# Optimization experiments

Measured on AMD Instinct MI355X. Metric: run time of the kernel, lower is better.

## Reference

```python
import jax, jax.numpy as jnp
import numpy as np

B, T, D, H, TE = 8, 1024, 1024, 16, 2048  # batch, seq, latent_dim, heads, time_embed_dim
LN_EPS = 1e-5


def layer_norm(x, w, b):
    m = jnp.mean(x, axis=-1, keepdims=True)
    v = jnp.var(x, axis=-1, keepdims=True)
    return (x - m) / jnp.sqrt(v + LN_EPS) * w + b


def setup_inputs() -> dict:
    key = jax.random.key(0)
    ks = jax.random.split(key, 8)
    s = lambda k, sh: (jax.random.normal(k, sh, jnp.float32) * 0.02)
    return dict(
        x=jax.random.normal(ks[0], (B, T, D), jnp.float32),
        emb=jax.random.normal(ks[1], (B, TE), jnp.float32),
        src_mask=jnp.ones((B, T), jnp.float32),
        norm_w=jnp.ones((D,), jnp.float32), norm_b=jnp.zeros((D,), jnp.float32),
        q_w=s(ks[2], (D, D)), q_b=jnp.zeros((D,), jnp.float32),
        k_w=s(ks[3], (D, D)), k_b=jnp.zeros((D,), jnp.float32),
        v_w=s(ks[4], (D, D)), v_b=jnp.zeros((D,), jnp.float32),
        emb_w=s(ks[5], (TE, 2 * D)), emb_b=jnp.zeros((2 * D,), jnp.float32),
        sb_norm_w=jnp.ones((D,), jnp.float32), sb_norm_b=jnp.zeros((D,), jnp.float32),
        out_w=s(ks[6], (D, D)), out_b=jnp.zeros((D,), jnp.float32),
    )


def reference(x, emb, src_mask, norm_w, norm_b, q_w, q_b, k_w, k_b, v_w, v_b,
              emb_w, emb_b, sb_norm_w, sb_norm_b, out_w, out_b):
    Bx, Tx, Dx = x.shape
    # the torch module applies the SAME LayerNorm to x three times; compute once
    xn = layer_norm(x, norm_w, norm_b)                      # [B,T,D]
    q = (xn @ q_w + q_b).reshape(Bx, Tx, H, -1)             # [B,T,H,l]
    k = (xn @ k_w + k_b).reshape(Bx, Tx, H, -1)
    att = jnp.einsum('bnhl,bmhl->bnmh', q, k)               # [B,T,T,H] (no 1/sqrt(d) scaling, as in source)
    mask = src_mask.reshape(Bx, 1, Tx, 1)
    att = att + (1.0 - mask) * -1000000.0
    att = jax.nn.softmax(att, axis=2)                       # softmax over keys (dim m)
    v = ((xn @ v_w + v_b) * src_mask[:, :, None]).reshape(Bx, Tx, H, -1)
    y = jnp.einsum('bnmh,bmhl->bnhl', att, v).reshape(Bx, Tx, Dx)
    # StylizationBlock (dropout is identity in eval)
    e = jax.nn.silu(emb) @ emb_w + emb_b                    # [B,2D]
    scale, shift = jnp.split(e[:, None, :], 2, axis=2)      # each [B,1,D]
    h = layer_norm(y, sb_norm_w, sb_norm_b) * (1.0 + scale) + shift
    h = jax.nn.silu(h) @ out_w + out_b
    return x + h
```

## Files before the change

### kernel.cpp

```cpp
#include <hip/hip_runtime.h>
#include <cstddef>
#include <cstdint>

#define B_SZ 8
#define T_SEQ 1024
#define D_MODEL 1024
#define NH 16
#define HD 64
#define TE_DIM 2048
#define BT_ROWS 8192

typedef short bf16x8 __attribute__((ext_vector_type(8)));
typedef float f32x4 __attribute__((ext_vector_type(4)));

#define MFMA16(a, b, c) __builtin_amdgcn_mfma_f32_16x16x32_bf16(a, b, c, 0, 0, 0)
#define EXP2(x) __builtin_amdgcn_exp2f(x)

__device__ inline unsigned short f2b(float f) {
  union { float f; unsigned u; } v; v.f = f;
  unsigned r = v.u + 0x7FFF + ((v.u >> 16) & 1);
  return (unsigned short)(r >> 16);
}

__device__ inline float b2f(unsigned short u) {
  union { unsigned u; float f; } v; v.u = ((unsigned)u) << 16; return v.f;
}

__device__ inline unsigned cvtpk(float a, float b) {
  unsigned r;
  asm("v_cvt_pk_bf16_f32 %0, %1, %2" : "=v"(r) : "v"(a), "v"(b));
  return r;
}

__device__ inline void gll16(const void* g, void* l) {
  __builtin_amdgcn_global_load_lds(
      (const __attribute__((address_space(1))) unsigned int*)g,
      (__attribute__((address_space(3))) unsigned int*)l, 16, 0, 0);
}

__global__ __launch_bounds__(256) void ln_kernel(
    const float* __restrict__ x, const float* __restrict__ w,
    const float* __restrict__ b, unsigned short* __restrict__ out)
{
  __shared__ float red[8];
  int row = blockIdx.x;
  int tid = threadIdx.x;
  const float* xr = x + (size_t)row * D_MODEL;
  float4 xv = *(const float4*)&xr[tid * 4];
  float s  = xv.x + xv.y + xv.z + xv.w;
  float ss = xv.x*xv.x + xv.y*xv.y + xv.z*xv.z + xv.w*xv.w;
  #pragma unroll
  for (int off = 32; off; off >>= 1) {
    s  += __shfl_xor(s, off);
    ss += __shfl_xor(ss, off);
  }
  int wv = tid >> 6;
  if ((tid & 63) == 0) { red[wv] = s; red[4 + wv] = ss; }
  __syncthreads();
  s  = red[0] + red[1] + red[2] + red[3];
  ss = red[4] + red[5] + red[6] + red[7];
  float mean = s * (1.f / D_MODEL);
  float var  = ss * (1.f / D_MODEL) - mean * mean;
  float inv  = rsqrtf(var + 1e-5f);
  float4 w4 = *(const float4*)&w[tid * 4];
  float4 b4 = *(const float4*)&b[tid * 4];
  ushort4 o;
  o.x = f2b((xv.x - mean) * inv * w4.x + b4.x);
  o.y = f2b((xv.y - mean) * inv * w4.y + b4.y);
  o.z = f2b((xv.z - mean) * inv * w4.z + b4.z);
  o.w = f2b((xv.w - mean) * inv * w4.w + b4.w);
  int kg = tid >> 4, cb = (tid >> 1) & 7, e = (tid & 1) * 4;
  int col = kg * 64 + ((cb ^ (row & 7)) * 8) + e;
  *(ushort4*)&out[(size_t)row * D_MODEL + col] = o;
}

__global__ __launch_bounds__(256) void transpose_w4(
    const float* __restrict__ s0, const float* __restrict__ s1,
    const float* __restrict__ s2, const float* __restrict__ s3,
    unsigned short* __restrict__ d0, unsigned short* __restrict__ d1,
    unsigned short* __restrict__ d2, unsigned short* __restrict__ d3)
{
  __shared__ float s[32][33];
  int z = blockIdx.z;
  const float* in = z == 0 ? s0 : z == 1 ? s1 : z == 2 ? s2 : s3;
  unsigned short* out = z == 0 ? d0 : z == 1 ? d1 : z == 2 ? d2 : d3;
  int tx = threadIdx.x & 31, ty = threadIdx.x >> 5;
  int r0 = blockIdx.y * 32, c0 = blockIdx.x * 32;
  #pragma unroll
  for (int rr = 0; rr < 4; ++rr)
    s[ty + rr * 8][tx] = in[(size_t)(r0 + ty + rr * 8) * D_MODEL + c0 + tx];
  __syncthreads();
  int k = r0 + tx;
  int kg = k >> 6, cb = (k >> 3) & 7, e = k & 7;
  #pragma unroll
  for (int rr = 0; rr < 4; ++rr) {
    int n = c0 + ty + rr * 8;
    int col = kg * 64 + ((cb ^ (n & 7)) * 8) + e;
    out[(size_t)n * D_MODEL + col] = f2b(s[tx][ty + rr * 8]);
  }
}

template <int MODE>
__global__ __launch_bounds__(512, 2) void gemm8(
    const unsigned short* __restrict__ A, const unsigned short* __restrict__ W,
    const float* __restrict__ b0, const float* __restrict__ b1,
    const float* __restrict__ b2, const float* __restrict__ mask,
    const float* __restrict__ resid, void* __restrict__ C)
{
  const int K = 1024;
  __shared__ __align__(16) unsigned short SA[3][256 * 64];
  __shared__ __align__(16) unsigned short SB[3][128 * 64];
  int tid = threadIdx.x;
  int wid = tid >> 6, lane = tid & 63, g = lane >> 4, lq = lane & 15;
  int wm = wid >> 1, wn = wid & 1;
  int bid = blockIdx.x;
  int xcd = bid & 7, ii = bid >> 3;
  int mt = xcd * 4 + (ii & 3), nt = ii >> 2;
  int m0 = mt * 256;
  int wg = (MODE == 1) ? (nt >> 3) : 0;
  int n0 = (MODE == 1) ? ((nt & 7) * 128) : (nt * 128);
  const unsigned short* Bt = W + ((size_t)wg << 20);
  const float* bias = (MODE == 1) ? (wg == 0 ? b0 : wg == 1 ? b1 : b2) : b0;

  f32x4 acc[4][4];
  #pragma unroll
  for (int i = 0; i < 4; ++i)
    #pragma unroll
    for (int j = 0; j < 4; ++j)
      acc[i][j] = (f32x4){0.f, 0.f, 0.f, 0.f};

  const unsigned short* aSrc = A + (size_t)(m0 + (tid >> 3)) * K + (tid & 7) * 8;
  const unsigned short* bSrc = Bt + (size_t)(n0 + (tid >> 3)) * K + (tid & 7) * 8;

  #define STAGE8(slot, t)                                                      \
    {                                                                          \
      size_t ko = (size_t)(t) * 64;                                            \
      _Pragma("unroll")                                                        \
      for (int i2 = 0; i2 < 4; ++i2)                                           \
        gll16(aSrc + ko + (size_t)i2 * 64 * K,                                 \
              (char*)&SA[slot][0] + tid * 16 + i2 * 8192);                     \
      _Pragma("unroll")                                                        \
      for (int i2 = 0; i2 < 2; ++i2)                                           \
        gll16(bSrc + ko + (size_t)i2 * 64 * K,                                 \
              (char*)&SB[slot][0] + tid * 16 + i2 * 8192);                     \
    }

  STAGE8(0, 0)
  STAGE8(1, 1)
  asm volatile("s_waitcnt vmcnt(6)" ::: "memory");
  asm volatile("s_barrier" ::: "memory");

  int cA0 = (g ^ (lq & 7)) * 16;
  int cA1 = ((4 + g) ^ (lq & 7)) * 16;

  #pragma unroll
  for (int t = 0; t < 16; ++t) {
    const char* sa = (const char*)&SA[t % 3][0];
    const char* sb = (const char*)&SB[t % 3][0];
    bf16x8 af[4][2], bf[4][2];
    #pragma unroll
    for (int i = 0; i < 4; ++i) {
      int ra = wm * 64 + i * 16 + lq;
      af[i][0] = *(const bf16x8*)(sa + ra * 128 + cA0);
      af[i][1] = *(const bf16x8*)(sa + ra * 128 + cA1);
      int rb = wn * 64 + i * 16 + lq;
      bf[i][0] = *(const bf16x8*)(sb + rb * 128 + cA0);
      bf[i][1] = *(const bf16x8*)(sb + rb * 128 + cA1);
    }
    if (t < 14) {
      STAGE8((t + 2) % 3, t + 2)
      asm volatile("s_waitcnt vmcnt(6)" ::: "memory");
    } else if (t == 14) {
      asm volatile("s_waitcnt vmcnt(0)" ::: "memory");
    }
    __builtin_amdgcn_s_setprio(1);
    #pragma unroll
    for (int i = 0; i < 4; ++i)
      #pragma unroll
      for (int j = 0; j < 4; ++j) {
        acc[i][j] = MFMA16(af[i][0], bf[j][0], acc[i][j]);
        acc[i][j] = MFMA16(af[i][1], bf[j][1], acc[i][j]);
      }
    __builtin_amdgcn_s_setprio(0);
    if (t < 15) asm volatile("s_barrier" ::: "memory");
  }
  #undef STAGE8

  int colbase = n0 + wn * 64;
  #pragma unroll
  for (int i = 0; i < 4; ++i) {
    int mrow0 = m0 + wm * 64 + i * 16 + g * 4;
    #pragma unroll
    for (int j = 0; j < 4; ++j) {
      int n = colbase + j * 16 + lq;
      float bv = bias[n];
      if (MODE == 0) {
        float* Cf = (float*)C;
        #pragma unroll
        for (int rr = 0; rr < 4; ++rr) {
          int m = mrow0 + rr;
          Cf[(size_t)m * D_MODEL + n] = acc[i][j][rr] + bv + resid[(size_t)m * D_MODEL + n];
        }
      } else {
        int h = n >> 6, dd = n & 63;
        unsigned short* O = (unsigned short*)C;
        if (wg < 2) {
          float scale = wg == 0 ? 1.44269504f : 1.0f;
          unsigned short* Cb = O + ((size_t)wg << 23);
          #pragma unroll
          for (int rr = 0; rr < 4; ++rr) {
            int m = mrow0 + rr;
            int b = m >> 10, tt = m & 1023;
            Cb[((size_t)((b * NH + h) * T_SEQ + tt)) * HD + dd] = f2b((acc[i][j][rr] + bv) * scale);
          }
        } else {
          unsigned short* Cb = O + ((size_t)2 << 23);
          int b = mrow0 >> 10, tt = mrow0 & 1023;
          ushort4 pk;
          unsigned short* pp = (unsigned short*)&pk;
          #pragma unroll
          for (int rr = 0; rr < 4; ++rr)
            pp[rr] = f2b((acc[i][j][rr] + bv) * mask[mrow0 + rr]);
          *(ushort4*)&Cb[((size_t)((b * NH + h) * HD + dd)) * T_SEQ + tt] = pk;
        }
      }
    }
  }
}

__global__ __launch_bounds__(256) void emb_partial(
    const float* __restrict__ emb, const float* __restrict__ emb_w,
    float* __restrict__ partial)
{
  __shared__ float ses[B_SZ][32];
  int tid = threadIdx.x;
  int t0 = blockIdx.y * 32;
  int n = blockIdx.x * 1024 + tid * 4;
  {
    int b = tid >> 5, t = tid & 31;
    float v = emb[b * TE_DIM + t0 + t];
    ses[b][t] = v / (1.f + __expf(-v));
  }
  __syncthreads();
  f32x4 acc[B_SZ];
  #pragma unroll
  for (int b = 0; b < B_SZ; ++b) acc[b] = (f32x4){0.f, 0.f, 0.f, 0.f};
  #pragma unroll 4
  for (int t = 0; t < 32; ++t) {
    f32x4 wv = *(const f32x4*)&emb_w[(size_t)(t0 + t) * (2 * D_MODEL) + n];
    #pragma unroll
    for (int b = 0; b < B_SZ; ++b) {
      float s = ses[b][t];
      acc[b][0] = fmaf(s, wv[0], acc[b][0]);
      acc[b][1] = fmaf(s, wv[1], acc[b][1]);
      acc[b][2] = fmaf(s, wv[2], acc[b][2]);
      acc[b][3] = fmaf(s, wv[3], acc[b][3]);
    }
  }
  #pragma unroll
  for (int b = 0; b < B_SZ; ++b)
    *(f32x4*)&partial[((size_t)blockIdx.y * B_SZ + b) * (2 * D_MODEL) + n] = acc[b];
}

__global__ __launch_bounds__(256) void emb_reduce(
    const float* __restrict__ partial, const float* __restrict__ emb_b,
    float* __restrict__ e)
{
  int idx = blockIdx.x * 256 + threadIdx.x;
  int b = idx >> 11, n = idx & 2047;
  float acc = emb_b[n];
  #pragma unroll 8
  for (int kb = 0; kb < 64; ++kb)
    acc += partial[((size_t)kb * B_SZ + b) * (2 * D_MODEL) + n];
  e[b * (2 * D_MODEL) + n] = acc;
}

__global__ __launch_bounds__(256, 2) void attn_mfma6(
    const unsigned short* __restrict__ Q, const unsigned short* __restrict__ K,
    const unsigned short* __restrict__ Vt, const float* __restrict__ mask,
    unsigned short* __restrict__ y)
{
  __shared__ __align__(16) unsigned short SM[32768];
  unsigned short* Kb = SM;
  unsigned short* Vb = SM + 8192;
  unsigned short* Pb = SM + 16384;

  int tid = threadIdx.x, w = tid >> 6, lane = tid & 63;
  int g = lane >> 4, lq = lane & 15;
  int bid = blockIdx.x;
  int lid = (bid & 7) * 64 + (bid >> 3);
  int qb = lid & 3, h = (lid >> 2) & 15, b = lid >> 6;
  int q0 = qb * 256 + w * 64;
  size_t hb = ((size_t)(b * NH + h)) * T_SEQ * HD;

  bf16x8 bq[4][2];
  #pragma unroll
  for (int qa = 0; qa < 4; ++qa)
    #pragma unroll
    for (int kh = 0; kh < 2; ++kh)
      bq[qa][kh] = *(const bf16x8*)(Q + hb + (size_t)(q0 + qa * 16 + lq) * HD + kh * 32 + g * 8);

  const char* kBase = (const char*)(K + hb) + lq * 128 + g * 16;
  const char* vBase = (const char*)(Vt + hb) + lq * 2048 + g * 16;
  int c0 = 2 * w, c1 = 2 * w + 1;
  const char* kS0 = kBase + (c0 >> 1) * 2048 + (c0 & 1) * 64;
  const char* kS1 = kBase + (c1 >> 1) * 2048 + (c1 & 1) * 64;
  const char* vS0 = vBase + (c0 >> 1) * 32768 + (c0 & 1) * 64;
  const char* vS1 = vBase + (c1 >> 1) * 32768 + (c1 & 1) * 64;

  f32x4 o[4][4];
  #pragma unroll
  for (int dt = 0; dt < 4; ++dt)
    #pragma unroll
    for (int qa = 0; qa < 4; ++qa)
      o[dt][qa] = (f32x4){0.f, 0.f, 0.f, 0.f};
  float mrun[4] = {-3.0e38f, -3.0e38f, -3.0e38f, -3.0e38f};
  float lrun[4] = {0.f, 0.f, 0.f, 0.f};
  const float* maskb = mask + b * T_SEQ;

  gll16(kS0, Kb + c0 * 512);
  gll16(kS1, Kb + c1 * 512);
  gll16(vS0, Vb + c0 * 512);
  gll16(vS1, Vb + c1 * 512);
  __syncthreads();

  for (int t = 0; t < 16; ++t) {
    int cur = t & 1;
    int kv0 = t * 64;
    if (t < 15) {
      int nxt = cur ^ 1;
      size_t ko = (size_t)(kv0 + 64) * 128;
      size_t vo = (size_t)(kv0 + 64) * 2;
      gll16(kS0 + ko, Kb + nxt * 4096 + c0 * 512);
      gll16(kS1 + ko, Kb + nxt * 4096 + c1 * 512);
      gll16(vS0 + vo, Vb + nxt * 4096 + c0 * 512);
      gll16(vS1 + vo, Vb + nxt * 4096 + c1 * 512);
    }
    const unsigned short* Kc = Kb + cur * 4096;
    const unsigned short* Vc = Vb + cur * 4096;

    bf16x8 kf[4][2];
    #pragma unroll
    for (int kt = 0; kt < 4; ++kt)
      #pragma unroll
      for (int kh = 0; kh < 2; ++kh)
        kf[kt][kh] = *(const bf16x8*)(Kc + (kt * 2 + kh) * 512 + lane * 8);

    f32x4 st[4][4];
    #pragma unroll
    for (int kt = 0; kt < 4; ++kt)
      #pragma unroll
      for (int qa = 0; qa < 4; ++qa)
        st[kt][qa] = (f32x4){0.f, 0.f, 0.f, 0.f};

    __builtin_amdgcn_s_setprio(1);
    #pragma unroll
    for (int kt = 0; kt < 4; ++kt)
      #pragma unroll
      for (int qa = 0; qa < 4; ++qa) {
        st[kt][qa] = MFMA16(kf[kt][0], bq[qa][0], st[kt][qa]);
        st[kt][qa] = MFMA16(kf[kt][1], bq[qa][1], st[kt][qa]);
      }
    __builtin_amdgcn_s_setprio(0);

    bf16x8 vf[4][2];
    #pragma unroll
    for (int dt = 0; dt < 4; ++dt)
      #pragma unroll
      for (int kh = 0; kh < 2; ++kh)
        vf[dt][kh] = *(const bf16x8*)(Vc + (dt * 2 + kh) * 512 + lane * 8);

    #pragma unroll
    for (int kt = 0; kt < 4; ++kt) {
      float4 mk = *(const float4*)&maskb[kv0 + kt * 16 + g * 4];
      float mb[4] = {(1.f - mk.x) * -1500000.f, (1.f - mk.y) * -1500000.f,
                     (1.f - mk.z) * -1500000.f, (1.f - mk.w) * -1500000.f};
      #pragma unroll
      for (int qa = 0; qa < 4; ++qa)
        #pragma unroll
        for (int r = 0; r < 4; ++r)
          st[kt][qa][r] += mb[r];
    }

    float tmax[4];
    #pragma unroll
    for (int qa = 0; qa < 4; ++qa) {
      float tm = st[0][qa][0];
      #pragma unroll
      for (int kt = 0; kt < 4; ++kt)
        #pragma unroll
        for (int r = 0; r < 4; ++r)
          tm = fmaxf(tm, st[kt][qa][r]);
      tm = fmaxf(tm, __shfl_xor(tm, 16));
      tm = fmaxf(tm, __shfl_xor(tm, 32));
      tmax[qa] = tm;
    }
    bool need = false;
    #pragma unroll
    for (int qa = 0; qa < 4; ++qa) need = need || (tmax[qa] > mrun[qa] + 11.5f);
    if (__any((int)need)) {
      #pragma unroll
      for (int qa = 0; qa < 4; ++qa) {
        float mnew = fmaxf(mrun[qa], tmax[qa]);
        float corr = EXP2(mrun[qa] - mnew);
        lrun[qa] *= corr;
        #pragma unroll
        for (int dt = 0; dt < 4; ++dt) {
          o[dt][qa][0] *= corr; o[dt][qa][1] *= corr;
          o[dt][qa][2] *= corr; o[dt][qa][3] *= corr;
        }
        mrun[qa] = mnew;
      }
    }
    #pragma unroll
    for (int qa = 0; qa < 4; ++qa) {
      float psum = 0.f;
      #pragma unroll
      for (int kt = 0; kt < 4; ++kt)
        #pragma unroll
        for (int r = 0; r < 4; ++r) {
          float p = EXP2(st[kt][qa][r] - mrun[qa]);
          st[kt][qa][r] = p;
          psum += p;
        }
      psum += __shfl_xor(psum, 16);
      psum += __shfl_xor(psum, 32);
      lrun[qa] += psum;
    }

    #pragma unroll
    for (int qa = 0; qa < 4; ++qa) {
      unsigned short* Pq = Pb + (w * 4 + qa) * 1024;
      #pragma unroll
      for (int kt = 0; kt < 4; ++kt) {
        uint2 pk2;
        pk2.x = cvtpk(st[kt][qa][0], st[kt][qa][1]);
        pk2.y = cvtpk(st[kt][qa][2], st[kt][qa][3]);
        *(uint2*)((char*)Pq + lq * 128 +
                  (((kt * 2 + (g >> 1)) ^ (lq & 7)) * 16) + (g & 1) * 8) = pk2;
      }
    }

    __builtin_amdgcn_s_setprio(1);
    #pragma unroll
    for (int qa = 0; qa < 4; ++qa) {
      const unsigned short* Pq = Pb + (w * 4 + qa) * 1024;
      #pragma unroll
      for (int kh = 0; kh < 2; ++kh) {
        bf16x8 pa = *(const bf16x8*)((const char*)Pq + lq * 128 +
                                     (((kh * 4 + g) ^ (lq & 7)) * 16));
        #pragma unroll
        for (int dt = 0; dt < 4; ++dt)
          o[dt][qa] = MFMA16(vf[dt][kh], pa, o[dt][qa]);
      }
    }
    __builtin_amdgcn_s_setprio(0);

    __syncthreads();
  }

  unsigned short* sc = SM + w * 4096;
  #pragma unroll
  for (int qa = 0; qa < 4; ++qa) {
    float inv = 1.f / lrun[qa];
    #pragma unroll
    for (int dt = 0; dt < 4; ++dt) {
      uint2 pk;
      pk.x = cvtpk(o[dt][qa][0] * inv, o[dt][qa][1] * inv);
      pk.y = cvtpk(o[dt][qa][2] * inv, o[dt][qa][3] * inv);
      *(uint2*)(sc + (qa * 16 + lq) * 64 + dt * 16 + g * 4) = pk;
    }
  }
  #pragma unroll
  for (int it = 0; it < 16; ++it) {
    int row = it * 4 + g;
    ushort4 v = *(const ushort4*)(sc + row * 64 + lq * 4);
    *(ushort4*)&y[(size_t)(b * T_SEQ + q0 + row) * D_MODEL + h * HD + lq * 4] = v;
  }
}

__global__ __launch_bounds__(256) void ln2_kernel(
    const unsigned short* __restrict__ y, const float* __restrict__ w,
    const float* __restrict__ b, const float* __restrict__ e,
    unsigned short* __restrict__ gout)
{
  __shared__ float red[8];
  int row = blockIdx.x;
  int tid = threadIdx.x;
  int bb = row >> 10;
  ushort4 u = *(const ushort4*)&y[(size_t)row * D_MODEL + tid * 4];
  float4 yv = {b2f(u.x), b2f(u.y), b2f(u.z), b2f(u.w)};
  float s  = yv.x + yv.y + yv.z + yv.w;
  float ss = yv.x*yv.x + yv.y*yv.y + yv.z*yv.z + yv.w*yv.w;
  #pragma unroll
  for (int off = 32; off; off >>= 1) {
    s  += __shfl_xor(s, off);
    ss += __shfl_xor(ss, off);
  }
  int wv = tid >> 6;
  if ((tid & 63) == 0) { red[wv] = s; red[4 + wv] = ss; }
  __syncthreads();
  s  = red[0] + red[1] + red[2] + red[3];
  ss = red[4] + red[5] + red[6] + red[7];
  float mean = s * (1.f / D_MODEL);
  float var  = ss * (1.f / D_MODEL) - mean * mean;
  float inv  = rsqrtf(var + 1e-5f);
  float vals[4] = {yv.x, yv.y, yv.z, yv.w};
  ushort4 o;
  unsigned short* op = (unsigned short*)&o;
  #pragma unroll
  for (int j = 0; j < 4; j++) {
    int c = tid * 4 + j;
    float val = (vals[j] - mean) * inv * w[c] + b[c];
    float sc = e[bb * (2 * D_MODEL) + c];
    float sh = e[bb * (2 * D_MODEL) + D_MODEL + c];
    val = val * (1.f + sc) + sh;
    op[j] = f2b(val / (1.f + __expf(-val)));
  }
  int kg = tid >> 4, cb = (tid >> 1) & 7, ee = (tid & 1) * 4;
  int col = kg * 64 + ((cb ^ (row & 7)) * 8) + ee;
  *(ushort4*)&gout[(size_t)row * D_MODEL + col] = o;
}

extern "C" void kernel_launch(void* const* d_in, const int* in_sizes, int n_in,
                              void* d_out, int out_size, void* d_ws, size_t ws_size,
                              hipStream_t stream) {
  const float* x      = (const float*)d_in[0];
  const float* emb    = (const float*)d_in[1];
  const float* mask   = (const float*)d_in[2];
  const float* norm_w = (const float*)d_in[3];
  const float* norm_b = (const float*)d_in[4];
  const float* q_w    = (const float*)d_in[5];
  const float* q_b    = (const float*)d_in[6];
  const float* k_w    = (const float*)d_in[7];
  const float* k_b    = (const float*)d_in[8];
  const float* v_w    = (const float*)d_in[9];
  const float* v_b    = (const float*)d_in[10];
  const float* emb_w  = (const float*)d_in[11];
  const float* emb_b  = (const float*)d_in[12];
  const float* sb_w   = (const float*)d_in[13];
  const float* sb_b   = (const float*)d_in[14];
  const float* out_w  = (const float*)d_in[15];
  const float* out_b  = (const float*)d_in[16];
  float* out = (float*)d_out;

  char* ws = (char*)d_ws;
  const size_t MB = 1u << 20;
  unsigned short* xn   = (unsigned short*)(ws);
  unsigned short* qkv  = (unsigned short*)(ws + 16 * MB);
  unsigned short* qb   = qkv;
  unsigned short* kb   = qkv + (1u << 23);
  unsigned short* vt   = qkv + (2u << 23);
  unsigned short* yb   = (unsigned short*)(ws + 64 * MB);
  unsigned short* gb   = (unsigned short*)(ws + 96 * MB);
  float*          ep   = (float*)(ws + 96 * MB);
  unsigned short* w3t  = (unsigned short*)(ws + 112 * MB);
  unsigned short* owt  = (unsigned short*)(ws + 118 * MB);
  float*          eb   = (float*)(ws + 120 * MB);

  transpose_w4<<<dim3(32, 32, 4), 256, 0, stream>>>(
      q_w, k_w, v_w, out_w,
      w3t, w3t + (1u << 20), w3t + (2u << 20), owt);

  ln_kernel<<<BT_ROWS, 256, 0, stream>>>(x, norm_w, norm_b, xn);

  gemm8<1><<<768, 512, 0, stream>>>(xn, w3t, q_b, k_b, v_b, mask, nullptr, qkv);

  emb_partial<<<dim3(2, 64), 256, 0, stream>>>(emb, emb_w, ep);
  emb_reduce<<<64, 256, 0, stream>>>(ep, emb_b, eb);

  attn_mfma6<<<512, 256, 0, stream>>>(qb, kb, vt, mask, yb);

  ln2_kernel<<<BT_ROWS, 256, 0, stream>>>(yb, sb_w, sb_b, eb, gb);

  gemm8<0><<<256, 512, 0, stream>>>(gb, owt, out_b, nullptr, nullptr, nullptr, x, out);
}
```

Baseline: 200.9 us.

## Fold mask into MFMA accumulator, compute row sums via MFMA, add dedicated out-proj GEMM

The attention kernel now seeds the QK MFMA accumulator with the mask bias instead of adding it afterwards. Softmax row sums are computed by an extra MFMA against a ones vector rather than VALU adds and cross-lane shuffles, and the max reduction uses three-input max. The output projection gets a separate simpler 128x128-tile GEMM with 512 blocks of 256 threads instead of the templated 256x128 kernel, which aims for better occupancy on the small N. The trade is extra MFMA work per tile and a single-buffered out GEMM with no prefetch overlap.

Result: faster. 193.5 us (median of 2 runs) (-3.7%).

```diff
diff --git a/kernel.cpp b/kernel.cpp
--- a/kernel.cpp
+++ b/kernel.cpp
@@ -30,6 +30,10 @@
   unsigned r;
   asm("v_cvt_pk_bf16_f32 %0, %1, %2" : "=v"(r) : "v"(a), "v"(b));
   return r;
+}
+
+__device__ inline float max3f(float a, float b, float c) {
+  return fmaxf(fmaxf(a, b), c);
 }
 
 __device__ inline void gll16(const void* g, void* l) {
@@ -100,12 +104,11 @@
   }
 }
 
-template <int MODE>
-__global__ __launch_bounds__(512, 2) void gemm8(
+__global__ __launch_bounds__(512, 2) void gemm_qkv8(
     const unsigned short* __restrict__ A, const unsigned short* __restrict__ W,
     const float* __restrict__ b0, const float* __restrict__ b1,
     const float* __restrict__ b2, const float* __restrict__ mask,
-    const float* __restrict__ resid, void* __restrict__ C)
+    unsigned short* __restrict__ O)
 {
   const int K = 1024;
   __shared__ __align__(16) unsigned short SA[3][256 * 64];
@@ -117,10 +120,10 @@
   int xcd = bid & 7, ii = bid >> 3;
   int mt = xcd * 4 + (ii & 3), nt = ii >> 2;
   int m0 = mt * 256;
-  int wg = (MODE == 1) ? (nt >> 3) : 0;
-  int n0 = (MODE == 1) ? ((nt & 7) * 128) : (nt * 128);
+  int wg = nt >> 3;
+  int n0 = (nt & 7) * 128;
   const unsigned short* Bt = W + ((size_t)wg << 20);
-  const float* bias = (MODE == 1) ? (wg == 0 ? b0 : wg == 1 ? b1 : b2) : b0;
+  const float* bias = wg == 0 ? b0 : wg == 1 ? b1 : b2;
 
   f32x4 acc[4][4];
   #pragma unroll
@@ -194,35 +197,97 @@
     for (int j = 0; j < 4; ++j) {
       int n = colbase + j * 16 + lq;
       float bv = bias[n];
-      if (MODE == 0) {
-        float* Cf = (float*)C;
+      int h = n >> 6, dd = n & 63;
+      if (wg < 2) {
+        float scale = wg == 0 ? 1.44269504f : 1.0f;
+        unsigned short* Cb = O + ((size_t)wg << 23);
         #pragma unroll
         for (int rr = 0; rr < 4; ++rr) {
           int m = mrow0 + rr;
-          Cf[(size_t)m * D_MODEL + n] = acc[i][j][rr] + bv + resid[(size_t)m * D_MODEL + n];
+          int b = m >> 10, tt = m & 1023;
+          Cb[((size_t)((b * NH + h) * T_SEQ + tt)) * HD + dd] = f2b((acc[i][j][rr] + bv) * scale);
         }
       } else {
-        int h = n >> 6, dd = n & 63;
-        unsigned short* O = (unsigned short*)C;
-        if (wg < 2) {
-          float scale = wg == 0 ? 1.44269504f : 1.0f;
-          unsigned short* Cb = O + ((size_t)wg << 23);
-          #pragma unroll
-          for (int rr = 0; rr < 4; ++rr) {
-            int m = mrow0 + rr;
-            int b = m >> 10, tt = m & 1023;
-            Cb[((size_t)((b * NH + h) * T_SEQ + tt)) * HD + dd] = f2b((acc[i][j][rr] + bv) * scale);
-          }
-        } else {
-          unsigned short* Cb = O + ((size_t)2 << 23);
-          int b = mrow0 >> 10, tt = mrow0 & 1023;
-          ushort4 pk;
-          unsigned short* pp = (unsigned short*)&pk;
-          #pragma unroll
-          for (int rr = 0; rr < 4; ++rr)
-            pp[rr] = f2b((acc[i][j][rr] + bv) * mask[mrow0 + rr]);
-          *(ushort4*)&Cb[((size_t)((b * NH + h) * HD + dd)) * T_SEQ + tt] = pk;
-        }
+        unsigned short* Cb = O + ((size_t)2 << 23);
+        int b = mrow0 >> 10, tt = mrow0 & 1023;
+        ushort4 pk;
+        unsigned short* pp = (unsigned short*)&pk;
+        #pragma unroll
+        for (int rr = 0; rr < 4; ++rr)
+          pp[rr] = f2b((acc[i][j][rr] + bv) * mask[mrow0 + rr]);
+        *(ushort4*)&Cb[((size_t)((b * NH + h) * HD + dd)) * T_SEQ + tt] = pk;
+      }
+    }
+  }
+}
+
+__global__ __launch_bounds__(256) void gemm_out(
+    const unsigned short* __restrict__ A, const unsigned short* __restrict__ Bt,
+    const float* __restrict__ bias, const float* __restrict__ resid,
+    float* __restrict__ C)
+{
+  const int K = 1024;
+  __shared__ __align__(16) unsigned short As[128 * 64];
+  __shared__ __align__(16) unsigned short Bs[128 * 64];
+  int l = blockIdx.x;
+  int xcd = l & 7, ii = l >> 3;
+  int mt = xcd * 8 + (ii & 7), nt = ii >> 3;
+  int m0 = mt * 128, n0 = nt * 128;
+
+  int tid = threadIdx.x;
+  int lane = tid & 63, w = tid >> 6;
+  int g = lane >> 4, lq = lane & 15;
+  int wr = w >> 1, wc = w & 1;
+  f32x4 acc[4][4];
+  #pragma unroll
+  for (int i = 0; i < 4; ++i)
+    #pragma unroll
+    for (int j = 0; j < 4; ++j)
+      acc[i][j] = (f32x4){0.f, 0.f, 0.f, 0.f};
+
+  const unsigned short* aSrc = A + (size_t)(m0 + (tid >> 3)) * K + (tid & 7) * 8;
+  const unsigned short* bSrc = Bt + (size_t)(n0 + (tid >> 3)) * K + (tid & 7) * 8;
+  char* aDst = (char*)As + tid * 16;
+  char* bDst = (char*)Bs + tid * 16;
+
+  for (int k0 = 0; k0 < K; k0 += 64) {
+    #pragma unroll
+    for (int it = 0; it < 4; ++it) {
+      gll16(aSrc + k0 + it * 32 * K, aDst + it * 4096);
+      gll16(bSrc + k0 + it * 32 * K, bDst + it * 4096);
+    }
+    __syncthreads();
+    #pragma unroll
+    for (int kh = 0; kh < 2; ++kh) {
+      bf16x8 af[4], bfr[4];
+      #pragma unroll
+      for (int i = 0; i < 4; ++i) {
+        int ra = wr * 64 + i * 16 + lq;
+        af[i] = *(const bf16x8*)((const char*)As + ra * 128 + (((kh * 4 + g) ^ (ra & 7)) * 16));
+        int rb = wc * 64 + i * 16 + lq;
+        bfr[i] = *(const bf16x8*)((const char*)Bs + rb * 128 + (((kh * 4 + g) ^ (rb & 7)) * 16));
+      }
+      #pragma unroll
+      for (int i = 0; i < 4; ++i)
+        #pragma unroll
+        for (int j = 0; j < 4; ++j)
+          acc[i][j] = MFMA16(af[i], bfr[j], acc[i][j]);
+    }
+    __syncthreads();
+  }
+
+  int colbase = n0 + wc * 64;
+  #pragma unroll
+  for (int i = 0; i < 4; ++i) {
+    int mrow0 = m0 + wr * 64 + i * 16 + g * 4;
+    #pragma unroll
+    for (int j = 0; j < 4; ++j) {
+      int n = colbase + j * 16 + lq;
+      float bv = bias[n];
+      #pragma unroll
+      for (int rr = 0; rr < 4; ++rr) {
+        int m = mrow0 + rr;
+        C[(size_t)m * D_MODEL + n] = acc[i][j][rr] + bv + resid[(size_t)m * D_MODEL + n];
       }
     }
   }
@@ -275,7 +340,7 @@
   e[b * (2 * D_MODEL) + n] = acc;
 }
 
-__global__ __launch_bounds__(256, 2) void attn_mfma6(
+__global__ __launch_bounds__(256, 2) void attn_mfma7(
     const unsigned short* __restrict__ Q, const unsigned short* __restrict__ K,
     const unsigned short* __restrict__ Vt, const float* __restrict__ mask,
     unsigned short* __restrict__ y)
@@ -300,6 +365,10 @@
     for (int kh = 0; kh < 2; ++kh)
       bq[qa][kh] = *(const bf16x8*)(Q + hb + (size_t)(q0 + qa * 16 + lq) * HD + kh * 32 + g * 8);
 
+  bf16x8 ones;
+  #pragma unroll
+  for (int i = 0; i < 8; ++i) ones[i] = (short)16256;
+
   const char* kBase = (const char*)(K + hb) + lq * 128 + g * 16;
   const char* vBase = (const char*)(Vt + hb) + lq * 2048 + g * 16;
   int c0 = 2 * w, c1 = 2 * w + 1;
@@ -309,13 +378,15 @@
   const char* vS1 = vBase + (c1 >> 1) * 32768 + (c1 & 1) * 64;
 
   f32x4 o[4][4];
-  #pragma unroll
-  for (int dt = 0; dt < 4; ++dt)
-    #pragma unroll
-    for (int qa = 0; qa < 4; ++qa)
+  f32x4 osum[4];
+  #pragma unroll
+  for (int qa = 0; qa < 4; ++qa) {
+    osum[qa] = (f32x4){0.f, 0.f, 0.f, 0.f};
+    #pragma unroll
+    for (int dt = 0; dt < 4; ++dt)
       o[dt][qa] = (f32x4){0.f, 0.f, 0.f, 0.f};
+  }
   float mrun[4] = {-3.0e38f, -3.0e38f, -3.0e38f, -3.0e38f};
-  float lrun[4] = {0.f, 0.f, 0.f, 0.f};
   const float* maskb = mask + b * T_SEQ;
 
   gll16(kS0, Kb + c0 * 512);
@@ -339,6 +410,16 @@
     const unsigned short* Kc = Kb + cur * 4096;
     const unsigned short* Vc = Vb + cur * 4096;
 
+    f32x4 mbv[4];
+    #pragma unroll
+    for (int kt = 0; kt < 4; ++kt) {
+      float4 mk = *(const float4*)&maskb[kv0 + kt * 16 + g * 4];
+      mbv[kt][0] = fmaf(mk.x, 1500000.f, -1500000.f);
+      mbv[kt][1] = fmaf(mk.y, 1500000.f, -1500000.f);
+      mbv[kt][2] = fmaf(mk.z, 1500000.f, -1500000.f);
+      mbv[kt][3] = fmaf(mk.w, 1500000.f, -1500000.f);
+    }
+
     bf16x8 kf[4][2];
     #pragma unroll
     for (int kt = 0; kt < 4; ++kt)
@@ -347,18 +428,12 @@
         kf[kt][kh] = *(const bf16x8*)(Kc + (kt * 2 + kh) * 512 + lane * 8);
 
     f32x4 st[4][4];
+    __builtin_amdgcn_s_setprio(1);
     #pragma unroll
     for (int kt = 0; kt < 4; ++kt)
       #pragma unroll
-      for (int qa = 0; qa < 4; ++qa)
-        st[kt][qa] = (f32x4){0.f, 0.f, 0.f, 0.f};
-
-    __builtin_amdgcn_s_setprio(1);
-    #pragma unroll
-    for (int kt = 0; kt < 4; ++kt)
-      #pragma unroll
       for (int qa = 0; qa < 4; ++qa) {
-        st[kt][qa] = MFMA16(kf[kt][0], bq[qa][0], st[kt][qa]);
+        st[kt][qa] = MFMA16(kf[kt][0], bq[qa][0], mbv[kt]);
         st[kt][qa] = MFMA16(kf[kt][1], bq[qa][1], st[kt][qa]);
       }
     __builtin_amdgcn_s_setprio(0);
@@ -370,27 +445,17 @@
       for (int kh = 0; kh < 2; ++kh)
         vf[dt][kh] = *(const bf16x8*)(Vc + (dt * 2 + kh) * 512 + lane * 8);
 
-    #pragma unroll
-    for (int kt = 0; kt < 4; ++kt) {
-      float4 mk = *(const float4*)&maskb[kv0 + kt * 16 + g * 4];
-      float mb[4] = {(1.f - mk.x) * -1500000.f, (1.f - mk.y) * -1500000.f,
-                     (1.f - mk.z) * -1500000.f, (1.f - mk.w) * -1500000.f};
-      #pragma unroll
-      for (int qa = 0; qa < 4; ++qa)
-        #pragma unroll
-        for (int r = 0; r < 4; ++r)
-          st[kt][qa][r] += mb[r];
-    }
-
     float tmax[4];
     #pragma unroll
     for (int qa = 0; qa < 4; ++qa) {
-      float tm = st[0][qa][0];
-      #pragma unroll
-      for (int kt = 0; kt < 4; ++kt)
-        #pragma unroll
-        for (int r = 0; r < 4; ++r)
-          tm = fmaxf(tm, st[kt][qa][r]);
+      float m0v = max3f(st[0][qa][0], st[0][qa][1], st[0][qa][2]);
+      float m1v = max3f(st[0][qa][3], st[1][qa][0], st[1][qa][1]);
+      float m2v = max3f(st[1][qa][2], st[1][qa][3], st[2][qa][0]);
+      float m3v = max3f(st[2][qa][1], st[2][qa][2], st[2][qa][3]);
+      float m4v = max3f(st[3][qa][0], st[3][qa][1], st[3][qa][2]);
+      float t0v = max3f(m0v, m1v, st[3][qa][3]);
+      float t1v = max3f(m2v, m3v, m4v);
+      float tm = fmaxf(t0v, t1v);
       tm = fmaxf(tm, __shfl_xor(tm, 16));
       tm = fmaxf(tm, __shfl_xor(tm, 32));
       tmax[qa] = tm;
@@ -403,7 +468,8 @@
       for (int qa = 0; qa < 4; ++qa) {
         float mnew = fmaxf(mrun[qa], tmax[qa]);
         float corr = EXP2(mrun[qa] - mnew);
-        lrun[qa] *= corr;
+        osum[qa][0] *= corr; osum[qa][1] *= corr;
+        osum[qa][2] *= corr; osum[qa][3] *= corr;
         #pragma unroll
         for (int dt = 0; dt < 4; ++dt) {
           o[dt][qa][0] *= corr; o[dt][qa][1] *= corr;
@@ -413,20 +479,12 @@
       }
     }
     #pragma unroll
-    for (int qa = 0; qa < 4; ++qa) {
-      float psum = 0.f;
+    for (int qa = 0; qa < 4; ++qa)
       #pragma unroll
       for (int kt = 0; kt < 4; ++kt)
         #pragma unroll
-        for (int r = 0; r < 4; ++r) {
-          float p = EXP2(st[kt][qa][r] - mrun[qa]);
-          st[kt][qa][r] = p;
-          psum += p;
-        }
-      psum += __shfl_xor(psum, 16);
-      psum += __shfl_xor(psum, 32);
-      lrun[qa] += psum;
-    }
+        for (int r = 0; r < 4; ++r)
+          st[kt][qa][r] = EXP2(st[kt][qa][r] - mrun[qa]);
 
     #pragma unroll
     for (int qa = 0; qa < 4; ++qa) {
@@ -449,6 +507,7 @@
       for (int kh = 0; kh < 2; ++kh) {
         bf16x8 pa = *(const bf16x8*)((const char*)Pq + lq * 128 +
                                      (((kh * 4 + g) ^ (lq & 7)) * 16));
+        osum[qa] = MFMA16(ones, pa, osum[qa]);
         #pragma unroll
         for (int dt = 0; dt < 4; ++dt)
           o[dt][qa] = MFMA16(vf[dt][kh], pa, o[dt][qa]);
@@ -462,7 +521,7 @@
   unsigned short* sc = SM + w * 4096;
   #pragma unroll
   for (int qa = 0; qa < 4; ++qa) {
-    float inv = 1.f / lrun[qa];
+    float inv = 1.f / osum[qa][0];
     #pragma unroll
     for (int dt = 0; dt < 4; ++dt) {
       uint2 pk;
@@ -564,14 +623,14 @@
 
   ln_kernel<<<BT_ROWS, 256, 0, stream>>>(x, norm_w, norm_b, xn);
 
-  gemm8<1><<<768, 512, 0, stream>>>(xn, w3t, q_b, k_b, v_b, mask, nullptr, qkv);
+  gemm_qkv8<<<768, 512, 0, stream>>>(xn, w3t, q_b, k_b, v_b, mask, qkv);
 
   emb_partial<<<dim3(2, 64), 256, 0, stream>>>(emb, emb_w, ep);
   emb_reduce<<<64, 256, 0, stream>>>(ep, emb_b, eb);
 
-  attn_mfma6<<<512, 256, 0, stream>>>(qb, kb, vt, mask, yb);
+  attn_mfma7<<<512, 256, 0, stream>>>(qb, kb, vt, mask, yb);
 
   ln2_kernel<<<BT_ROWS, 256, 0, stream>>>(yb, sb_w, sb_b, eb, gb);
 
-  gemm8<0><<<256, 512, 0, stream>>>(gb, owt, out_b, nullptr, nullptr, nullptr, x, out);
-}
+  gemm_out<<<512, 256, 0, stream>>>(gb, owt, out_b, x, out);
+}
```
